# Optimization experiments

Hardware: AMD Instinct MI355X
Metric: run time of the kernel (lower is better)

## Reference

```python
import jax, jax.numpy as jnp
import numpy as np

E, N = 400000, 50000
D = 128          # efeat_dim = src_dim = dst_dim = output_dim
H = 512          # hidden_dim
CAT = 3 * D      # concat of [efeat, src, dst]
LN_EPS = 1e-5


def setup_inputs() -> dict:
    key = jax.random.key(0)
    ks = jax.random.split(key, 12)
    scale = 0.02
    return {
        "efeat": jax.random.normal(ks[0], (E, D), jnp.float32),
        "src_feat": jax.random.normal(ks[1], (N, D), jnp.float32),
        "dst_feat": jax.random.normal(ks[2], (N, D), jnp.float32),
        "src_idx": jax.random.randint(ks[3], (E,), 0, N),
        "dst_idx": jax.random.randint(ks[4], (E,), 0, N),
        # MLP params: Linear(CAT,H) -> SiLU -> Linear(H,H) -> SiLU -> Linear(H,D) -> LayerNorm(D)
        "W1": jax.random.normal(ks[5], (CAT, H), jnp.float32) * scale,
        "b1": jnp.zeros((H,), jnp.float32),
        "W2": jax.random.normal(ks[6], (H, H), jnp.float32) * scale,
        "b2": jnp.zeros((H,), jnp.float32),
        "W3": jax.random.normal(ks[7], (H, D), jnp.float32) * scale,
        "b3": jnp.zeros((D,), jnp.float32),
        "gamma": jnp.ones((D,), jnp.float32),
        "beta": jnp.zeros((D,), jnp.float32),
    }


def _layer_norm(y, gamma, beta):
    mu = jnp.mean(y, axis=-1, keepdims=True)
    var = jnp.mean(jnp.square(y - mu), axis=-1, keepdims=True)
    return (y - mu) * jax.lax.rsqrt(var + LN_EPS) * gamma + beta


def reference(efeat, src_feat, dst_feat, src_idx, dst_idx,
              W1, b1, W2, b2, W3, b3, gamma, beta):
    # concat_efeat: per-edge gather of src/dst node feats + concat with edge feats
    cat = jnp.concatenate([efeat, src_feat[src_idx], dst_feat[dst_idx]], axis=1)  # [E, 3D]
    h = jax.nn.silu(cat @ W1 + b1)   # [E, H]
    h = jax.nn.silu(h @ W2 + b2)     # [E, H]
    y = h @ W3 + b3                  # [E, D]
    return _layer_norm(y, gamma, beta)
```

## Files before the change

### kernel.cpp

```cpp
#include <hip/hip_runtime.h>
#include <hip/hip_bf16.h>
#include <cstdint>
#include <cstddef>

typedef __attribute__((ext_vector_type(4))) float f32x4;
typedef __attribute__((ext_vector_type(8))) short s16x8;

#define E_ 400000
#define D_ 128
#define H_ 512
#define CAT_ 384
#define BM 64
#define NBLK 6250

#define CATPITCH 40
#define CATSLOT (BM * CATPITCH * 2)
#define RINGBASE (65536 - 5 * CATSLOT)
#define LDS_TOTAL 65536

__device__ __forceinline__ unsigned short f2bf(float x) {
  union { float f; unsigned u; } t; t.f = x;
  return (unsigned short)((t.u + 0x8000u) >> 16);
}
__device__ __forceinline__ float silu_f(float x) {
  return x * __builtin_amdgcn_rcpf(1.0f + __expf(-x));
}

#define HS(row, byteoff) (smem + (row) * 1024 + ((byteoff) ^ (((row) & 7) << 4)))

__global__ __launch_bounds__(512, 4)
void edge_mlp_fused(const float* __restrict__ efeat,
                    const float* __restrict__ src_feat,
                    const float* __restrict__ dst_feat,
                    const int* __restrict__ src_idx,
                    const int* __restrict__ dst_idx,
                    const unsigned short* __restrict__ P1,
                    const unsigned short* __restrict__ P2,
                    const unsigned short* __restrict__ P3,
                    const float* __restrict__ b1,
                    const float* __restrict__ b2,
                    const float* __restrict__ b3,
                    const float* __restrict__ gamma,
                    const float* __restrict__ beta,
                    float* __restrict__ out) {
  extern __shared__ char smem[];
  const int tid = threadIdx.x;
  const int lane = tid & 63;
  const int wave = tid >> 6;
  const int lr = lane & 15;
  const int kc = lane >> 4;
  const int g4 = kc * 4;
  const size_t e0 = (size_t)blockIdx.x * BM;

  const int grow = tid >> 3, gq = tid & 7;
  const size_t ee = e0 + grow;
  const float* gb0 = efeat + ee * D_;
  const float* gb1 = src_feat + (size_t)src_idx[ee] * D_;
  const float* gb2 = dst_feat + (size_t)dst_idx[ee] * D_;
  f32x4 ga[2];

#define CGLOAD(P) { ga[(P) & 1] = *(const f32x4*)(((P) < 4 ? gb0 : (P) < 8 ? gb1 : gb2) + ((P) & 3) * 32 + gq * 4); }
#define CPWRITE(P) { unsigned short* d_ = (unsigned short*)(smem + RINGBASE + ((P) % 5) * CATSLOT) + grow * CATPITCH + gq * 4; \
                     const f32x4 v_ = ga[(P) & 1]; \
                     ushort4 w_; \
                     w_.x = f2bf(v_[0]); w_.y = f2bf(v_[1]); \
                     w_.z = f2bf(v_[2]); w_.w = f2bf(v_[3]); \
                     *(ushort4*)d_ = w_; }

  const unsigned short* w1base = P1 + (size_t)kc * 4096 + wave * 512 + lr * 8;
  const unsigned short* w2base = P2 + (size_t)kc * 4096 + wave * 512 + lr * 8;
  const unsigned short* w3base = P3 + (size_t)kc * 1024 + lr * 8;

  {
    f32x4 acc[4][4];
    #pragma unroll
    for (int eg = 0; eg < 4; ++eg)
      #pragma unroll
      for (int j = 0; j < 4; ++j) acc[eg][j] = (f32x4){0.f, 0.f, 0.f, 0.f};

    CGLOAD(0); CPWRITE(0);
    CGLOAD(1); CPWRITE(1);
    CGLOAD(2); CPWRITE(2);
    CGLOAD(3);

    asm volatile("s_waitcnt lgkmcnt(0)" ::: "memory");
    __builtin_amdgcn_s_barrier();
    asm volatile("" ::: "memory");

    #pragma unroll
    for (int p = 0; p < 12; ++p) {
      s16x8 w[4];
      #pragma unroll
      for (int j = 0; j < 4; ++j)
        w[j] = *(const s16x8*)(w1base + (size_t)p * 16384 + j * 128);

      if (p <= 8) { CPWRITE(p + 3); if (p <= 7) CGLOAD(p + 4); }

      asm volatile("s_waitcnt lgkmcnt(0)" ::: "memory");
      __builtin_amdgcn_s_barrier();
      asm volatile("" ::: "memory");

      const unsigned short* cp = (const unsigned short*)(smem + RINGBASE + (p % 5) * CATSLOT);
      #pragma unroll
      for (int eg = 0; eg < 4; ++eg) {
        const s16x8 bf = *(const s16x8*)(cp + (eg * 16 + lr) * CATPITCH + kc * 8);
        #pragma unroll
        for (int j = 0; j < 4; ++j)
          acc[eg][j] = __builtin_amdgcn_mfma_f32_16x16x32_bf16(w[j], bf, acc[eg][j], 0, 0, 0);
      }
    }

    __builtin_amdgcn_s_barrier();
    asm volatile("" ::: "memory");

    #pragma unroll
    for (int j = 0; j < 4; ++j) {
      const int col0 = (wave * 4 + j) * 16 + g4;
      const f32x4 bv = *(const f32x4*)(b1 + col0);
      #pragma unroll
      for (int eg = 0; eg < 4; ++eg) {
        ushort4 w_;
        w_.x = f2bf(silu_f(acc[eg][j][0] + bv[0]));
        w_.y = f2bf(silu_f(acc[eg][j][1] + bv[1]));
        w_.z = f2bf(silu_f(acc[eg][j][2] + bv[2]));
        w_.w = f2bf(silu_f(acc[eg][j][3] + bv[3]));
        *(ushort4*)HS(eg * 16 + lr, col0 * 2) = w_;
      }
    }
  }
  __syncthreads();

  {
    f32x4 acc[4][4];
    #pragma unroll
    for (int eg = 0; eg < 4; ++eg)
      #pragma unroll
      for (int j = 0; j < 4; ++j) acc[eg][j] = (f32x4){0.f, 0.f, 0.f, 0.f};

    #pragma unroll
    for (int p = 0; p < 16; ++p) {
      s16x8 w[4];
      #pragma unroll
      for (int j = 0; j < 4; ++j)
        w[j] = *(const s16x8*)(w2base + (size_t)p * 16384 + j * 128);
      #pragma unroll
      for (int eg = 0; eg < 4; ++eg) {
        const s16x8 bf = *(const s16x8*)HS(eg * 16 + lr, p * 64 + kc * 16);
        #pragma unroll
        for (int j = 0; j < 4; ++j)
          acc[eg][j] = __builtin_amdgcn_mfma_f32_16x16x32_bf16(w[j], bf, acc[eg][j], 0, 0, 0);
      }
    }
    __syncthreads();

    #pragma unroll
    for (int j = 0; j < 4; ++j) {
      const int col0 = (wave * 4 + j) * 16 + g4;
      const f32x4 bv = *(const f32x4*)(b2 + col0);
      #pragma unroll
      for (int eg = 0; eg < 4; ++eg) {
        ushort4 w_;
        w_.x = f2bf(silu_f(acc[eg][j][0] + bv[0]));
        w_.y = f2bf(silu_f(acc[eg][j][1] + bv[1]));
        w_.z = f2bf(silu_f(acc[eg][j][2] + bv[2]));
        w_.w = f2bf(silu_f(acc[eg][j][3] + bv[3]));
        *(ushort4*)HS(eg * 16 + lr, col0 * 2) = w_;
      }
    }
  }
  __syncthreads();

  if (wave < 4) {
    f32x4 acc[8];
    #pragma unroll
    for (int f = 0; f < 8; ++f) acc[f] = (f32x4){0.f, 0.f, 0.f, 0.f};

    #pragma unroll
    for (int p = 0; p < 16; ++p) {
      s16x8 w[8];
      #pragma unroll
      for (int f = 0; f < 8; ++f)
        w[f] = *(const s16x8*)(w3base + (size_t)p * 4096 + f * 128);
      const s16x8 bf = *(const s16x8*)HS(wave * 16 + lr, p * 64 + kc * 16);
      #pragma unroll
      for (int f = 0; f < 8; ++f)
        acc[f] = __builtin_amdgcn_mfma_f32_16x16x32_bf16(w[f], bf, acc[f], 0, 0, 0);
    }

    const int edge = wave * 16 + lr;
    float sum = 0.f, ss = 0.f;
    #pragma unroll
    for (int f = 0; f < 8; ++f) {
      const f32x4 bv = *(const f32x4*)(b3 + f * 16 + g4);
      #pragma unroll
      for (int r = 0; r < 4; ++r) {
        acc[f][r] += bv[r];
        sum += acc[f][r];
        ss += acc[f][r] * acc[f][r];
      }
    }
    sum += __shfl_xor(sum, 16, 64); ss += __shfl_xor(ss, 16, 64);
    sum += __shfl_xor(sum, 32, 64); ss += __shfl_xor(ss, 32, 64);
    const float mu = sum * (1.0f / 128.0f);
    const float var = ss * (1.0f / 128.0f) - mu * mu;
    const float rstd = rsqrtf(var + 1e-5f);
    float* orow = out + (e0 + edge) * D_;
    #pragma unroll
    for (int f = 0; f < 8; ++f) {
      const f32x4 gv = *(const f32x4*)(gamma + f * 16 + g4);
      const f32x4 btv = *(const f32x4*)(beta + f * 16 + g4);
      f32x4 o;
      #pragma unroll
      for (int r = 0; r < 4; ++r)
        o[r] = (acc[f][r] - mu) * rstd * gv[r] + btv[r];
      *(f32x4*)(orow + f * 16 + g4) = o;
    }
  }
#undef CGLOAD
#undef CPWRITE
}

__global__ void prep_pack(const float* __restrict__ W, unsigned short* __restrict__ P,
                          int K, int N) {
  const int t = blockIdx.x * blockDim.x + threadIdx.x;
  if (t >= N * (K >> 3)) return;
  const int n = t % N;
  const int k8 = t / N;
  const int k0 = k8 << 3;
  const int p = k0 >> 5, kc = (k0 >> 3) & 3;
  s16x8 w;
  #pragma unroll
  for (int j = 0; j < 8; ++j)
    w[j] = (short)f2bf(W[(size_t)(k0 + j) * N + n]);
  *(s16x8*)(P + (size_t)p * N * 32 + (size_t)kc * N * 8 + (size_t)n * 8) = w;
}

extern "C" void kernel_launch(void* const* d_in, const int* in_sizes, int n_in,
                              void* d_out, int out_size, void* d_ws, size_t ws_size,
                              hipStream_t stream) {
  const float* efeat    = (const float*)d_in[0];
  const float* src_feat = (const float*)d_in[1];
  const float* dst_feat = (const float*)d_in[2];
  const int*   src_idx  = (const int*)d_in[3];
  const int*   dst_idx  = (const int*)d_in[4];
  const float* W1 = (const float*)d_in[5];
  const float* b1 = (const float*)d_in[6];
  const float* W2 = (const float*)d_in[7];
  const float* b2 = (const float*)d_in[8];
  const float* W3 = (const float*)d_in[9];
  const float* b3 = (const float*)d_in[10];
  const float* gamma = (const float*)d_in[11];
  const float* beta  = (const float*)d_in[12];

  unsigned short* P1 = (unsigned short*)d_ws;
  unsigned short* P2 = P1 + 196608;
  unsigned short* P3 = P2 + 262144;

  (void)hipFuncSetAttribute((const void*)edge_mlp_fused,
                            hipFuncAttributeMaxDynamicSharedMemorySize, LDS_TOTAL);

  prep_pack<<<(512 * 48 + 255) / 256, 256, 0, stream>>>(W1, P1, CAT_, H_);
  prep_pack<<<(512 * 64 + 255) / 256, 256, 0, stream>>>(W2, P2, H_, H_);
  prep_pack<<<(128 * 64 + 255) / 256, 256, 0, stream>>>(W3, P3, H_, D_);

  edge_mlp_fused<<<NBLK, 512, LDS_TOTAL, stream>>>(
      efeat, src_feat, dst_feat, src_idx, dst_idx,
      P1, P2, P3, b1, b2, b3, gamma, beta, (float*)d_out);
}
```

Measured before the change: 572.0 us.

## Stage full concat tile in LDS upfront and drop per-step ring barriers

After: 625.5 us. 9.3% more time.

```diff
diff --git a/kernel.cpp b/kernel.cpp
--- a/kernel.cpp
+++ b/kernel.cpp
@@ -12,10 +12,6 @@
 #define CAT_ 384
 #define BM 64
 #define NBLK 6250
-
-#define CATPITCH 40
-#define CATSLOT (BM * CATPITCH * 2)
-#define RINGBASE (65536 - 5 * CATSLOT)
 #define LDS_TOTAL 65536
 
 __device__ __forceinline__ unsigned short f2bf(float x) {
@@ -52,58 +48,52 @@
   const int g4 = kc * 4;
   const size_t e0 = (size_t)blockIdx.x * BM;
 
-  const int grow = tid >> 3, gq = tid & 7;
-  const size_t ee = e0 + grow;
-  const float* gb0 = efeat + ee * D_;
-  const float* gb1 = src_feat + (size_t)src_idx[ee] * D_;
-  const float* gb2 = dst_feat + (size_t)dst_idx[ee] * D_;
-  f32x4 ga[2];
-
-#define CGLOAD(P) { ga[(P) & 1] = *(const f32x4*)(((P) < 4 ? gb0 : (P) < 8 ? gb1 : gb2) + ((P) & 3) * 32 + gq * 4); }
-#define CPWRITE(P) { unsigned short* d_ = (unsigned short*)(smem + RINGBASE + ((P) % 5) * CATSLOT) + grow * CATPITCH + gq * 4; \
-                     const f32x4 v_ = ga[(P) & 1]; \
-                     ushort4 w_; \
-                     w_.x = f2bf(v_[0]); w_.y = f2bf(v_[1]); \
-                     w_.z = f2bf(v_[2]); w_.w = f2bf(v_[3]); \
-                     *(ushort4*)d_ = w_; }
-
   const unsigned short* w1base = P1 + (size_t)kc * 4096 + wave * 512 + lr * 8;
   const unsigned short* w2base = P2 + (size_t)kc * 4096 + wave * 512 + lr * 8;
   const unsigned short* w3base = P3 + (size_t)kc * 1024 + lr * 8;
 
   {
+    const int row = tid >> 3, gq = tid & 7;
+    const size_t ee = e0 + row;
+    const float* bases[3];
+    bases[0] = efeat + ee * D_;
+    bases[1] = src_feat + (size_t)src_idx[ee] * D_;
+    bases[2] = dst_feat + (size_t)dst_idx[ee] * D_;
+    #pragma unroll
+    for (int s = 0; s < 3; ++s) {
+      #pragma unroll
+      for (int i = 0; i < 2; ++i) {
+        const float* sp = bases[s] + i * 64 + gq * 8;
+        const f32x4 v0 = *(const f32x4*)sp;
+        const f32x4 v1 = *(const f32x4*)(sp + 4);
+        s16x8 w_;
+        w_[0] = f2bf(v0[0]); w_[1] = f2bf(v0[1]); w_[2] = f2bf(v0[2]); w_[3] = f2bf(v0[3]);
+        w_[4] = f2bf(v1[0]); w_[5] = f2bf(v1[1]); w_[6] = f2bf(v1[2]); w_[7] = f2bf(v1[3]);
+        const int colb = (s * 128 + i * 64 + gq * 8) * 2;
+        *(s16x8*)HS(row, colb) = w_;
+      }
+    }
+  }
+  asm volatile("s_waitcnt lgkmcnt(0)" ::: "memory");
+  __builtin_amdgcn_s_barrier();
+  asm volatile("" ::: "memory");
+
+  {
     f32x4 acc[4][4];
     #pragma unroll
     for (int eg = 0; eg < 4; ++eg)
       #pragma unroll
       for (int j = 0; j < 4; ++j) acc[eg][j] = (f32x4){0.f, 0.f, 0.f, 0.f};
 
-    CGLOAD(0); CPWRITE(0);
-    CGLOAD(1); CPWRITE(1);
-    CGLOAD(2); CPWRITE(2);
-    CGLOAD(3);
-
-    asm volatile("s_waitcnt lgkmcnt(0)" ::: "memory");
-    __builtin_amdgcn_s_barrier();
-    asm volatile("" ::: "memory");
-
-    #pragma unroll
+    #pragma unroll 2
     for (int p = 0; p < 12; ++p) {
       s16x8 w[4];
       #pragma unroll
       for (int j = 0; j < 4; ++j)
         w[j] = *(const s16x8*)(w1base + (size_t)p * 16384 + j * 128);
-
-      if (p <= 8) { CPWRITE(p + 3); if (p <= 7) CGLOAD(p + 4); }
-
-      asm volatile("s_waitcnt lgkmcnt(0)" ::: "memory");
-      __builtin_amdgcn_s_barrier();
-      asm volatile("" ::: "memory");
-
-      const unsigned short* cp = (const unsigned short*)(smem + RINGBASE + (p % 5) * CATSLOT);
-      #pragma unroll
-      for (int eg = 0; eg < 4; ++eg) {
-        const s16x8 bf = *(const s16x8*)(cp + (eg * 16 + lr) * CATPITCH + kc * 8);
+      #pragma unroll
+      for (int eg = 0; eg < 4; ++eg) {
+        const s16x8 bf = *(const s16x8*)HS(eg * 16 + lr, p * 64 + kc * 16);
         #pragma unroll
         for (int j = 0; j < 4; ++j)
           acc[eg][j] = __builtin_amdgcn_mfma_f32_16x16x32_bf16(w[j], bf, acc[eg][j], 0, 0, 0);
@@ -128,7 +118,9 @@
       }
     }
   }
-  __syncthreads();
+  asm volatile("s_waitcnt lgkmcnt(0)" ::: "memory");
+  __builtin_amdgcn_s_barrier();
+  asm volatile("" ::: "memory");
 
   {
     f32x4 acc[4][4];
@@ -137,7 +129,7 @@
       #pragma unroll
       for (int j = 0; j < 4; ++j) acc[eg][j] = (f32x4){0.f, 0.f, 0.f, 0.f};
 
-    #pragma unroll
+    #pragma unroll 2
     for (int p = 0; p < 16; ++p) {
       s16x8 w[4];
       #pragma unroll
@@ -151,7 +143,9 @@
           acc[eg][j] = __builtin_amdgcn_mfma_f32_16x16x32_bf16(w[j], bf, acc[eg][j], 0, 0, 0);
       }
     }
-    __syncthreads();
+
+    __builtin_amdgcn_s_barrier();
+    asm volatile("" ::: "memory");
 
     #pragma unroll
     for (int j = 0; j < 4; ++j) {
@@ -168,23 +162,28 @@
       }
     }
   }
-  __syncthreads();
+  asm volatile("s_waitcnt lgkmcnt(0)" ::: "memory");
+  __builtin_amdgcn_s_barrier();
+  asm volatile("" ::: "memory");
 
   if (wave < 4) {
     f32x4 acc[8];
     #pragma unroll
     for (int f = 0; f < 8; ++f) acc[f] = (f32x4){0.f, 0.f, 0.f, 0.f};
 
-    #pragma unroll
+    #pragma unroll 2
     for (int p = 0; p < 16; ++p) {
-      s16x8 w[8];
-      #pragma unroll
-      for (int f = 0; f < 8; ++f)
-        w[f] = *(const s16x8*)(w3base + (size_t)p * 4096 + f * 128);
       const s16x8 bf = *(const s16x8*)HS(wave * 16 + lr, p * 64 + kc * 16);
       #pragma unroll
-      for (int f = 0; f < 8; ++f)
-        acc[f] = __builtin_amdgcn_mfma_f32_16x16x32_bf16(w[f], bf, acc[f], 0, 0, 0);
+      for (int half = 0; half < 2; ++half) {
+        s16x8 w[4];
+        #pragma unroll
+        for (int j = 0; j < 4; ++j)
+          w[j] = *(const s16x8*)(w3base + (size_t)p * 4096 + half * 512 + j * 128);
+        #pragma unroll
+        for (int j = 0; j < 4; ++j)
+          acc[half * 4 + j] = __builtin_amdgcn_mfma_f32_16x16x32_bf16(w[j], bf, acc[half * 4 + j], 0, 0, 0);
+      }
     }
 
     const int edge = wave * 16 + lr;
@@ -216,8 +215,6 @@
       *(f32x4*)(orow + f * 16 + g4) = o;
     }
   }
-#undef CGLOAD
-#undef CPWRITE
 }
 
 __global__ void prep_pack(const float* __restrict__ W, unsigned short* __restrict__ P,
```
